# Kernel tuning notes

Measured on AMD Instinct MI355X. Metric: run time of the kernel, lower is better.

The kernel has to match this reference:

```python
import jax, jax.numpy as jnp
from jax import lax
import numpy as np

B, N, D = 2, 4096, 1024
D_INNER = 2 * D          # expand=2
D_STATE = 16
D_CONV = 4
DT_RANK = (D + 15) // 16 # ceil(d_model/16) = 64
EPS = 1e-6


def setup_inputs() -> dict:
    key = jax.random.key(0)
    ks = jax.random.split(key, 12)
    s = lambda k, shape, sc=0.02: jax.random.normal(k, shape, jnp.float32) * sc
    return {
        "x": jax.random.normal(ks[0], (B, N, D), jnp.float32),
        "c": jax.random.normal(ks[1], (B, D), jnp.float32),
        # LayerNorm(hidden_size, eps=1e-6)
        "ln_g": jnp.ones((D,), jnp.float32),
        "ln_b": jnp.zeros((D,), jnp.float32),
        # adaLN_modulation: SiLU -> Linear(D, 3D)
        "ada_w": s(ks[2], (3 * D, D)),
        "ada_b": jnp.zeros((3 * D,), jnp.float32),
        # Mamba params
        "in_w": s(ks[3], (2 * D_INNER, D)),                     # in_proj (no bias)
        "conv_w": s(ks[4], (D_INNER, 1, D_CONV), 0.1),          # depthwise causal conv
        "conv_b": jnp.zeros((D_INNER,), jnp.float32),
        "xproj_w": s(ks[5], (DT_RANK + 2 * D_STATE, D_INNER)),  # x_proj (no bias)
        "dt_w": s(ks[6], (D_INNER, DT_RANK), 0.1),              # dt_proj
        "dt_b": jnp.log(jnp.expm1(jnp.full((D_INNER,), 0.01, jnp.float32))),  # softplus^-1(0.01)
        "A_log": jnp.log(jnp.tile(jnp.arange(1, D_STATE + 1, dtype=jnp.float32), (D_INNER, 1))),
        "D_skip": jnp.ones((D_INNER,), jnp.float32),
        "out_w": s(ks[7], (D, D_INNER)),                        # out_proj (no bias)
    }


def _mamba(h, in_w, conv_w, conv_b, xproj_w, dt_w, dt_b, A_log, D_skip, out_w):
    Bsz = h.shape[0]
    xz = h @ in_w.T                                   # (B,N,2*Di)
    u, z = jnp.split(xz, 2, axis=-1)                  # (B,N,Di) each
    # causal depthwise conv over time
    u = u.transpose(0, 2, 1)                          # (B,Di,N)
    u = lax.conv_general_dilated(u, conv_w, (1,), [(D_CONV - 1, 0)],
                                 feature_group_count=D_INNER)
    u = jax.nn.silu(u + conv_b[None, :, None]).transpose(0, 2, 1)  # (B,N,Di)
    # input-dependent dt, B, C
    dbc = u @ xproj_w.T                               # (B,N,dt_rank+2S)
    dt = dbc[..., :DT_RANK]
    Bm = dbc[..., DT_RANK:DT_RANK + D_STATE]          # (B,N,S)
    Cm = dbc[..., DT_RANK + D_STATE:]                 # (B,N,S)
    dt = jax.nn.softplus(dt @ dt_w.T + dt_b)          # (B,N,Di)
    A = -jnp.exp(A_log)                               # (Di,S)

    def step(hst, inputs):
        dt_t, b_t, c_t, u_t = inputs                  # (B,Di),(B,S),(B,S),(B,Di)
        dA = jnp.exp(dt_t[..., None] * A)             # (B,Di,S)
        hst = dA * hst + (dt_t * u_t)[..., None] * b_t[:, None, :]
        y = jnp.einsum('bds,bs->bd', hst, c_t)
        return hst, y

    xs = (dt.transpose(1, 0, 2), Bm.transpose(1, 0, 2),
          Cm.transpose(1, 0, 2), u.transpose(1, 0, 2))
    h0 = jnp.zeros((Bsz, D_INNER, D_STATE), h.dtype)
    _, ys = lax.scan(step, h0, xs)                    # ys: (N,B,Di)
    y = ys.transpose(1, 0, 2) + u * D_skip            # D skip connection
    y = y * jax.nn.silu(z)                            # gate
    return y @ out_w.T                                # (B,N,D)


def reference(x, c, ln_g, ln_b, ada_w, ada_b, in_w, conv_w, conv_b,
              xproj_w, dt_w, dt_b, A_log, D_skip, out_w):
    # adaLN modulation
    mod = jax.nn.silu(c) @ ada_w.T + ada_b            # (B,3D)
    shift, scale, gate = jnp.split(mod, 3, axis=-1)
    # LayerNorm(eps=1e-6)
    mu = jnp.mean(x, axis=-1, keepdims=True)
    var = jnp.mean(jnp.square(x - mu), axis=-1, keepdims=True)
    h = (x - mu) * lax.rsqrt(var + EPS) * ln_g + ln_b
    # modulate
    h = h * (1.0 + scale[:, None, :]) + shift[:, None, :]
    # Mamba selective scan
    h = _mamba(h, in_w, conv_w, conv_b, xproj_w, dt_w, dt_b, A_log, D_skip, out_w)
    # gated residual
    return x + gate[:, None, :] * h
```

## Files before the change

### kernel.cpp

```cpp
#include <hip/hip_runtime.h>

typedef unsigned short u16;
typedef short s8v __attribute__((ext_vector_type(8)));
typedef short s4v __attribute__((ext_vector_type(4)));
typedef float f4v __attribute__((ext_vector_type(4)));

#define DEV __device__ __forceinline__

DEV float bf2f(u16 u) { union { unsigned i; float f; } x; x.i = ((unsigned)u) << 16; return x.f; }
DEV u16 f2bf(float f) {
  union { float f; unsigned i; } x; x.f = f;
  unsigned r = x.i + 0x7FFFu + ((x.i >> 16) & 1u);
  return (u16)(r >> 16);
}
DEV float sbf(short s) { return bf2f((u16)s); }
DEV float sigm(float v) { return 1.f / (1.f + __expf(-v)); }

DEV void gl_lds(const u16* g, u16* l) {
  __builtin_amdgcn_global_load_lds(
      (const __attribute__((address_space(1))) unsigned int*)g,
      (__attribute__((address_space(3))) unsigned int*)l, 16, 0, 0);
}

struct CvtArgs { const void* src[15]; u16* dst[15]; int n8[15]; };

__global__ __launch_bounds__(256)
void k_convert_all(CvtArgs a) {
  const int f32in = (((const unsigned*)a.src[2])[0] == 0x3F800000u);
#pragma unroll
  for (int s = 0; s < 15; ++s) {
    const int n8 = a.n8[s];
    const void* src = a.src[s];
    u16* dst = a.dst[s];
    for (int i = blockIdx.x * 256 + threadIdx.x; i < n8; i += gridDim.x * 256) {
      if (f32in) {
        const f4v* f = (const f4v*)src;
        f4v va = f[(size_t)i * 2], vb = f[(size_t)i * 2 + 1];
        s8v o;
#pragma unroll
        for (int e = 0; e < 4; ++e) { o[e] = (short)f2bf(va[e]); o[4 + e] = (short)f2bf(vb[e]); }
        *(s8v*)(dst + (size_t)i * 8) = o;
      } else {
        *(s8v*)(dst + (size_t)i * 8) = ((const s8v*)src)[i];
      }
    }
  }
}

__global__ __launch_bounds__(64)
void k_mod(const u16* __restrict__ c, const u16* __restrict__ ada_w,
           const u16* __restrict__ ada_b, float* __restrict__ mod) {
  int o = blockIdx.x;
  int b = o / 3072, col = o % 3072;
  int lane = threadIdx.x;
  float acc = 0.f;
  for (int k = lane; k < 1024; k += 64) {
    float cv = bf2f(c[b * 1024 + k]);
    acc += cv * sigm(cv) * bf2f(ada_w[(size_t)col * 1024 + k]);
  }
#pragma unroll
  for (int off = 1; off < 64; off <<= 1) acc += __shfl_xor(acc, off);
  if (lane == 0) mod[o] = acc + bf2f(ada_b[col]);
}

__global__ __launch_bounds__(256)
void k_ln(const u16* __restrict__ x, const u16* __restrict__ gw, const u16* __restrict__ bw,
          const float* __restrict__ mod, u16* __restrict__ h) {
  int m = blockIdx.x, tid = threadIdx.x;
  int b = m >> 12;
  s4v xv = *(const s4v*)(x + (size_t)m * 1024 + tid * 4);
  float v[4]; float sum = 0.f, sq = 0.f;
#pragma unroll
  for (int e = 0; e < 4; ++e) { v[e] = sbf(xv[e]); sum += v[e]; sq += v[e] * v[e]; }
#pragma unroll
  for (int off = 1; off < 64; off <<= 1) { sum += __shfl_xor(sum, off); sq += __shfl_xor(sq, off); }
  __shared__ float s1[4], s2[4];
  if ((tid & 63) == 0) { s1[tid >> 6] = sum; s2[tid >> 6] = sq; }
  __syncthreads();
  sum = s1[0] + s1[1] + s1[2] + s1[3];
  sq  = s2[0] + s2[1] + s2[2] + s2[3];
  float mu = sum * (1.f / 1024.f);
  float rs = rsqrtf(sq * (1.f / 1024.f) - mu * mu + 1e-6f);
  const float* mrow = mod + b * 3072;
  s4v o4;
#pragma unroll
  for (int e = 0; e < 4; ++e) {
    int col = tid * 4 + e;
    float hv = (v[e] - mu) * rs * sbf(gw[col]) + sbf(bw[col]);
    hv = hv * (1.f + mrow[1024 + col]) + mrow[col];
    o4[e] = (short)f2bf(hv);
  }
  *(s4v*)(h + (size_t)m * 1024 + tid * 4) = o4;
}

enum { EPI_SPLIT = 0, EPI_DT = 1, EPI_OUT = 2 };

template <int EPI>
__global__ __launch_bounds__(256)
void gemm_bt(const u16* __restrict__ A, const u16* __restrict__ W, int Kdim,
             u16* __restrict__ out0, u16* __restrict__ out1,
             const float* __restrict__ modp, const u16* __restrict__ xin,
             const u16* __restrict__ dtb, const unsigned* __restrict__ rawg) {
  __shared__ __align__(16) u16 As[128 * 32];
  __shared__ __align__(16) u16 Bs[128 * 32];
  const int tid = threadIdx.x;
  const int lane = tid & 63, wid = tid >> 6;
  const int tm = blockIdx.x * 128, tn = blockIdx.y * 128;
  const int wm = (wid >> 1) * 64, wn = (wid & 1) * 64;
  const int g = lane >> 4, r15 = lane & 15;
  const int r0 = tid >> 2, c0 = (tid & 3) << 3;
  int f32out = 0;
  if constexpr (EPI == EPI_OUT) f32out = (rawg[0] == 0x3F800000u);

  f4v zero = {0.f, 0.f, 0.f, 0.f};
  f4v acc[4][4];
#pragma unroll
  for (int i = 0; i < 4; ++i)
#pragma unroll
    for (int j = 0; j < 4; ++j) acc[i][j] = zero;

  for (int k0 = 0; k0 < Kdim; k0 += 32) {
    __syncthreads();
    gl_lds(A + (size_t)(tm + r0) * Kdim + k0 + c0, As + tid * 8);
    gl_lds(A + (size_t)(tm + r0 + 64) * Kdim + k0 + c0, As + 2048 + tid * 8);
    gl_lds(W + (size_t)(tn + r0) * Kdim + k0 + c0, Bs + tid * 8);
    gl_lds(W + (size_t)(tn + r0 + 64) * Kdim + k0 + c0, Bs + 2048 + tid * 8);
    __syncthreads();
    s8v af[4], bf[4];
#pragma unroll
    for (int f = 0; f < 4; ++f) {
      af[f] = *(const s8v*)(As + (wm + f * 16 + r15) * 32 + g * 8);
      bf[f] = *(const s8v*)(Bs + (wn + f * 16 + r15) * 32 + g * 8);
    }
#pragma unroll
    for (int i = 0; i < 4; ++i)
#pragma unroll
      for (int j = 0; j < 4; ++j)
        acc[i][j] = __builtin_amdgcn_mfma_f32_16x16x32_bf16(af[i], bf[j], acc[i][j], 0, 0, 0);
  }

#pragma unroll
  for (int i = 0; i < 4; ++i)
#pragma unroll
    for (int j = 0; j < 4; ++j)
#pragma unroll
      for (int r = 0; r < 4; ++r) {
        int m = tm + wm + i * 16 + g * 4 + r;
        int col = tn + wn + j * 16 + r15;
        float v = acc[i][j][r];
        if constexpr (EPI == EPI_SPLIT) {
          if (col < 2048) out0[(size_t)m * 2048 + col] = f2bf(v);
          else            out1[(size_t)m * 2048 + (col - 2048)] = f2bf(v);
        } else if constexpr (EPI == EPI_DT) {
          v += bf2f(dtb[col]);
          v = v > 20.f ? v : log1pf(__expf(v));
          out0[(size_t)m * 2048 + col] = f2bf(v);
        } else {
          int b = m >> 12;
          float gate = modp[b * 3072 + 2048 + col];
          float xv = bf2f(xin[(size_t)m * 1024 + col]);
          float res = xv + gate * v;
          if (f32out) ((float*)out0)[(size_t)m * 1024 + col] = res;
          else        out0[(size_t)m * 1024 + col] = f2bf(res);
        }
      }
}

__global__ __launch_bounds__(128)
void gemm_dbc(const u16* __restrict__ A, const u16* __restrict__ W,
              u16* __restrict__ dtin, float* __restrict__ bc) {
  __shared__ __align__(16) u16 As[32 * 32];
  __shared__ __align__(16) u16 Bs[96 * 32];
  const int tid = threadIdx.x;
  const int lane = tid & 63, wid = tid >> 6;
  const int tm = blockIdx.x * 32;
  const int g = lane >> 4, r15 = lane & 15;
  const int r0 = tid >> 2, c0 = (tid & 3) << 3;

  f4v zero = {0.f, 0.f, 0.f, 0.f};
  f4v acc[6];
#pragma unroll
  for (int j = 0; j < 6; ++j) acc[j] = zero;

  for (int k0 = 0; k0 < 2048; k0 += 32) {
    __syncthreads();
    gl_lds(A + (size_t)(tm + r0) * 2048 + k0 + c0, As + tid * 8);
    gl_lds(W + (size_t)r0 * 2048 + k0 + c0,        Bs + tid * 8);
    gl_lds(W + (size_t)(r0 + 32) * 2048 + k0 + c0, Bs + 1024 + tid * 8);
    gl_lds(W + (size_t)(r0 + 64) * 2048 + k0 + c0, Bs + 2048 + tid * 8);
    __syncthreads();
    s8v af = *(const s8v*)(As + (wid * 16 + r15) * 32 + g * 8);
    s8v bf[6];
#pragma unroll
    for (int f = 0; f < 6; ++f)
      bf[f] = *(const s8v*)(Bs + (f * 16 + r15) * 32 + g * 8);
#pragma unroll
    for (int j = 0; j < 6; ++j)
      acc[j] = __builtin_amdgcn_mfma_f32_16x16x32_bf16(af, bf[j], acc[j], 0, 0, 0);
  }

#pragma unroll
  for (int j = 0; j < 6; ++j)
#pragma unroll
    for (int r = 0; r < 4; ++r) {
      int m = tm + wid * 16 + g * 4 + r;
      int col = j * 16 + r15;
      float v = acc[j][r];
      if (col < 64) dtin[(size_t)m * 64 + col] = f2bf(v);
      else          bc[(size_t)m * 32 + (col - 64)] = v;
    }
}

#define TT 16
__global__ __launch_bounds__(256)
void k_conv(const u16* __restrict__ uraw, const u16* __restrict__ cw,
            const u16* __restrict__ cb, u16* __restrict__ uo) {
  const int b = blockIdx.y;
  const int t0 = blockIdx.x * TT;
  const int dbase = threadIdx.x * 8;
  const size_t rowbase = (size_t)b * 4096 + t0;

  s8v cwv[4];
#pragma unroll
  for (int q = 0; q < 4; ++q) cwv[q] = *(const s8v*)(cw + dbase * 4 + q * 8);
  float w[8][4];
#pragma unroll
  for (int e = 0; e < 8; ++e)
#pragma unroll
    for (int j = 0; j < 4; ++j) { int q = e * 4 + j; w[e][j] = sbf(cwv[q >> 3][q & 7]); }
  s8v cbv = *(const s8v*)(cb + dbase);
  float bias[8];
#pragma unroll
  for (int e = 0; e < 8; ++e) bias[e] = sbf(cbv[e]);

  s8v rows[TT + 3];
  const s8v zz = {0, 0, 0, 0, 0, 0, 0, 0};
#pragma unroll
  for (int r = 0; r < TT + 3; ++r) {
    int t = t0 - 3 + r;
    rows[r] = (t < 0) ? zz : *(const s8v*)(uraw + (rowbase - 3 + r) * 2048 + dbase);
  }

#pragma unroll
  for (int t = 0; t < TT; ++t) {
    float acc[8];
#pragma unroll
    for (int e = 0; e < 8; ++e) acc[e] = bias[e];
#pragma unroll
    for (int j = 0; j < 4; ++j) {
      s8v v = rows[t + j];
#pragma unroll
      for (int e = 0; e < 8; ++e) acc[e] = fmaf(sbf(v[e]), w[e][j], acc[e]);
    }
    s8v o;
#pragma unroll
    for (int e = 0; e < 8; ++e) { float s = acc[e]; o[e] = (short)f2bf(s * sigm(s)); }
    *(s8v*)(uo + (rowbase + t) * 2048 + dbase) = o;
  }
}

#define NC 32
#define CT 128

__global__ __launch_bounds__(256)
void scan_local(const u16* __restrict__ dt, const u16* __restrict__ u,
                const float* __restrict__ bc, const u16* __restrict__ A_log,
                float* __restrict__ P, float* __restrict__ F) {
  const int cch = blockIdx.x, b = blockIdx.z;
  const int tid = threadIdx.x;
  const int d = blockIdx.y * 256 + tid;
  __shared__ float lbc[CT * 32];
  const size_t mbase = (size_t)b * 4096 + (size_t)cch * CT;
  for (int i = tid; i < CT * 32; i += 256) lbc[i] = bc[mbase * 32 + i];
  float Ads[16];
#pragma unroll
  for (int s = 0; s < 16; ++s) Ads[s] = -__expf(bf2f(A_log[d * 16 + s]));
  float h[16];
#pragma unroll
  for (int s = 0; s < 16; ++s) h[s] = 0.f;
  float S = 0.f;
  __syncthreads();
  const u16* dtp = dt + mbase * 2048 + d;
  const u16* up  = u  + mbase * 2048 + d;
  for (int t = 0; t < CT; ++t) {
    float dtv = bf2f(dtp[(size_t)t * 2048]);
    float uv  = bf2f(up[(size_t)t * 2048]);
    float du = dtv * uv;
    S += dtv;
    float Bv[16];
    *(f4v*)&Bv[0]  = *(const f4v*)&lbc[t * 32 + 0];
    *(f4v*)&Bv[4]  = *(const f4v*)&lbc[t * 32 + 4];
    *(f4v*)&Bv[8]  = *(const f4v*)&lbc[t * 32 + 8];
    *(f4v*)&Bv[12] = *(const f4v*)&lbc[t * 32 + 12];
#pragma unroll
    for (int s = 0; s < 16; ++s) {
      float a = __expf(dtv * Ads[s]);
      h[s] = fmaf(a, h[s], du * Bv[s]);
    }
  }
  const size_t o = (((size_t)b * NC + cch) * 2048 + d) * 16;
#pragma unroll
  for (int q = 0; q < 4; ++q) {
    f4v fv, pv;
#pragma unroll
    for (int e = 0; e < 4; ++e) { fv[e] = h[q * 4 + e]; pv[e] = __expf(S * Ads[q * 4 + e]); }
    *(f4v*)&F[o + q * 4] = fv;
    *(f4v*)&P[o + q * 4] = pv;
  }
}

__global__ __launch_bounds__(256)
void scan_cross(float* __restrict__ P, float* __restrict__ F) {
  int tid = blockIdx.x * 256 + threadIdx.x;
  int b = tid >> 15, r = tid & 32767;
  float H = 0.f;
  for (int cc = 0; cc < NC; ++cc) {
    size_t o = (((size_t)b * NC + cc) << 15) + r;
    float Pv = P[o], Fv = F[o];
    F[o] = H;
    H = fmaf(Pv, H, Fv);
  }
}

__global__ __launch_bounds__(256)
void scan_final(const u16* __restrict__ dt, const u16* __restrict__ u,
                const float* __restrict__ bc, const u16* __restrict__ A_log,
                const float* __restrict__ Hin, const u16* __restrict__ z,
                const u16* __restrict__ Dskip, u16* __restrict__ Ain) {
  const int cch = blockIdx.x, b = blockIdx.z;
  const int tid = threadIdx.x;
  const int d = blockIdx.y * 256 + tid;
  __shared__ float lbc[CT * 32];
  const size_t mbase = (size_t)b * 4096 + (size_t)cch * CT;
  for (int i = tid; i < CT * 32; i += 256) lbc[i] = bc[mbase * 32 + i];
  float Ads[16];
#pragma unroll
  for (int s = 0; s < 16; ++s) Ads[s] = -__expf(bf2f(A_log[d * 16 + s]));
  float h[16];
  const size_t o = (((size_t)b * NC + cch) * 2048 + d) * 16;
#pragma unroll
  for (int q = 0; q < 4; ++q) {
    f4v hv = *(const f4v*)&Hin[o + q * 4];
#pragma unroll
    for (int e = 0; e < 4; ++e) h[q * 4 + e] = hv[e];
  }
  const float dsk = bf2f(Dskip[d]);
  __syncthreads();
  const u16* dtp = dt + mbase * 2048 + d;
  const u16* up  = u  + mbase * 2048 + d;
  const u16* zp  = z  + mbase * 2048 + d;
  u16* op = Ain + mbase * 2048 + d;
  for (int t = 0; t < CT; ++t) {
    float dtv = bf2f(dtp[(size_t)t * 2048]);
    float uv  = bf2f(up[(size_t)t * 2048]);
    float zv  = bf2f(zp[(size_t)t * 2048]);
    float du = dtv * uv;
    float Bv[16], Cv[16];
    *(f4v*)&Bv[0]  = *(const f4v*)&lbc[t * 32 + 0];
    *(f4v*)&Bv[4]  = *(const f4v*)&lbc[t * 32 + 4];
    *(f4v*)&Bv[8]  = *(const f4v*)&lbc[t * 32 + 8];
    *(f4v*)&Bv[12] = *(const f4v*)&lbc[t * 32 + 12];
    *(f4v*)&Cv[0]  = *(const f4v*)&lbc[t * 32 + 16];
    *(f4v*)&Cv[4]  = *(const f4v*)&lbc[t * 32 + 20];
    *(f4v*)&Cv[8]  = *(const f4v*)&lbc[t * 32 + 24];
    *(f4v*)&Cv[12] = *(const f4v*)&lbc[t * 32 + 28];
    float y = 0.f;
#pragma unroll
    for (int s = 0; s < 16; ++s) {
      float a = __expf(dtv * Ads[s]);
      h[s] = fmaf(a, h[s], du * Bv[s]);
      y = fmaf(h[s], Cv[s], y);
    }
    float zs = zv * sigm(zv);
    op[(size_t)t * 2048] = f2bf((y + uv * dsk) * zs);
  }
}

extern "C" void kernel_launch(void* const* d_in, const int* in_sizes, int n_in,
                              void* d_out, int out_size, void* d_ws, size_t ws_size,
                              hipStream_t stream) {
  u16* out = (u16*)d_out;

  char* ws = (char*)d_ws;
  size_t off = 0;
  auto alloc = [&](size_t bytes) { void* p = ws + off; off += (bytes + 255) & ~(size_t)255; return p; };
  u16* cv[15];
  for (int i = 0; i < 15; ++i) cv[i] = (u16*)alloc((size_t)in_sizes[i] * 2);
  float* mod   = (float*)alloc(2 * 3072 * 4);
  u16*   zbuf  = (u16*)  alloc((size_t)8192 * 2048 * 2);
  u16*   uraw  = (u16*)  alloc((size_t)8192 * 2048 * 2);
  u16*   uconv = (u16*)  alloc((size_t)8192 * 2048 * 2);
  u16*   dtin  = (u16*)  alloc((size_t)8192 * 64 * 2);
  float* bc    = (float*)alloc((size_t)8192 * 32 * 4);
  float* Pb    = (float*)alloc((size_t)2 * NC * 2048 * 16 * 4);
  float* Fb    = (float*)alloc((size_t)2 * NC * 2048 * 16 * 4);
  u16*   Ain   = (u16*)  alloc((size_t)8192 * 2048 * 2);
  u16*   hln   = Ain;
  u16*   dtbuf = uraw;

  CvtArgs ca;
  for (int i = 0; i < 15; ++i) { ca.src[i] = d_in[i]; ca.dst[i] = cv[i]; ca.n8[i] = in_sizes[i] / 8; }
  k_convert_all<<<2048, 256, 0, stream>>>(ca);

  const u16 *x = cv[0], *c = cv[1], *ada_w = cv[4],
            *ada_b = cv[5], *in_w = cv[6], *conv_w = cv[7], *conv_b = cv[8],
            *xproj = cv[9], *dt_w = cv[10], *dt_b = cv[11], *A_log = cv[12],
            *Dskip = cv[13], *out_w = cv[14];
  const u16 *ln_gb = cv[2], *ln_bb = cv[3];
  const unsigned* rawg = (const unsigned*)d_in[2];

  k_mod<<<6144, 64, 0, stream>>>(c, ada_w, ada_b, mod);
  k_ln<<<8192, 256, 0, stream>>>(x, ln_gb, ln_bb, mod, hln);
  gemm_bt<EPI_SPLIT><<<dim3(64, 32), 256, 0, stream>>>(hln, in_w, 1024, uraw, zbuf, nullptr, nullptr, nullptr, nullptr);
  k_conv<<<dim3(256, 2), 256, 0, stream>>>(uraw, conv_w, conv_b, uconv);
  gemm_dbc<<<256, 128, 0, stream>>>(uconv, xproj, dtin, bc);
  gemm_bt<EPI_DT><<<dim3(64, 16), 256, 0, stream>>>(dtin, dt_w, 64, dtbuf, nullptr, nullptr, nullptr, dt_b, nullptr);
  scan_local<<<dim3(NC, 8, 2), 256, 0, stream>>>(dtbuf, uconv, bc, A_log, Pb, Fb);
  scan_cross<<<256, 256, 0, stream>>>(Pb, Fb);
  scan_final<<<dim3(NC, 8, 2), 256, 0, stream>>>(dtbuf, uconv, bc, A_log, Fb, zbuf, Dskip, Ain);
  gemm_bt<EPI_OUT><<<dim3(64, 8), 256, 0, stream>>>(Ain, out_w, 2048, out, nullptr, mod, x, nullptr, rawg);
}
```

Baseline: 593.5 us.

## Double-buffer GEMM LDS tiles and read raw x directly instead of converting

Both MFMA GEMM kernels now use two LDS buffers, issuing the next K-tile's global-to-LDS loads before computing on the current tile, with one barrier per iteration instead of two. Separately, the conversion pass skips x, and the LayerNorm and output epilogue read the raw input (fp32 or bf16, detected from ln_g) directly. This removes an 8192x1024 conversion pass and overlaps load latency with MFMA work, at the cost of doubled LDS per block, which may reduce occupancy.

```diff
diff --git a/kernel.cpp b/kernel.cpp
--- a/kernel.cpp
+++ b/kernel.cpp
@@ -64,14 +64,25 @@
 }
 
 __global__ __launch_bounds__(256)
-void k_ln(const u16* __restrict__ x, const u16* __restrict__ gw, const u16* __restrict__ bw,
+void k_ln(const void* __restrict__ xraw, const unsigned* __restrict__ rawg,
+          const u16* __restrict__ gw, const u16* __restrict__ bw,
           const float* __restrict__ mod, u16* __restrict__ h) {
   int m = blockIdx.x, tid = threadIdx.x;
   int b = m >> 12;
-  s4v xv = *(const s4v*)(x + (size_t)m * 1024 + tid * 4);
-  float v[4]; float sum = 0.f, sq = 0.f;
-#pragma unroll
-  for (int e = 0; e < 4; ++e) { v[e] = sbf(xv[e]); sum += v[e]; sq += v[e] * v[e]; }
+  const int f32in = (rawg[0] == 0x3F800000u);
+  float v[4];
+  if (f32in) {
+    f4v xv = ((const f4v*)xraw)[(size_t)m * 256 + tid];
+#pragma unroll
+    for (int e = 0; e < 4; ++e) v[e] = xv[e];
+  } else {
+    s4v xv = ((const s4v*)xraw)[(size_t)m * 256 + tid];
+#pragma unroll
+    for (int e = 0; e < 4; ++e) v[e] = sbf(xv[e]);
+  }
+  float sum = 0.f, sq = 0.f;
+#pragma unroll
+  for (int e = 0; e < 4; ++e) { sum += v[e]; sq += v[e] * v[e]; }
 #pragma unroll
   for (int off = 1; off < 64; off <<= 1) { sum += __shfl_xor(sum, off); sq += __shfl_xor(sq, off); }
   __shared__ float s1[4], s2[4];
@@ -99,10 +110,10 @@
 __global__ __launch_bounds__(256)
 void gemm_bt(const u16* __restrict__ A, const u16* __restrict__ W, int Kdim,
              u16* __restrict__ out0, u16* __restrict__ out1,
-             const float* __restrict__ modp, const u16* __restrict__ xin,
+             const float* __restrict__ modp, const void* __restrict__ xin,
              const u16* __restrict__ dtb, const unsigned* __restrict__ rawg) {
-  __shared__ __align__(16) u16 As[128 * 32];
-  __shared__ __align__(16) u16 Bs[128 * 32];
+  __shared__ __align__(16) u16 As[2][128 * 32];
+  __shared__ __align__(16) u16 Bs[2][128 * 32];
   const int tid = threadIdx.x;
   const int lane = tid & 63, wid = tid >> 6;
   const int tm = blockIdx.x * 128, tn = blockIdx.y * 128;
@@ -112,6 +123,11 @@
   int f32out = 0;
   if constexpr (EPI == EPI_OUT) f32out = (rawg[0] == 0x3F800000u);
 
+  const u16* Ap  = A + (size_t)(tm + r0) * Kdim + c0;
+  const u16* Ap2 = A + (size_t)(tm + r0 + 64) * Kdim + c0;
+  const u16* Wp  = W + (size_t)(tn + r0) * Kdim + c0;
+  const u16* Wp2 = W + (size_t)(tn + r0 + 64) * Kdim + c0;
+
   f4v zero = {0.f, 0.f, 0.f, 0.f};
   f4v acc[4][4];
 #pragma unroll
@@ -119,24 +135,33 @@
 #pragma unroll
     for (int j = 0; j < 4; ++j) acc[i][j] = zero;
 
+  gl_lds(Ap, As[0] + tid * 8);
+  gl_lds(Ap2, As[0] + 2048 + tid * 8);
+  gl_lds(Wp, Bs[0] + tid * 8);
+  gl_lds(Wp2, Bs[0] + 2048 + tid * 8);
+  __syncthreads();
+
+  int cur = 0;
   for (int k0 = 0; k0 < Kdim; k0 += 32) {
-    __syncthreads();
-    gl_lds(A + (size_t)(tm + r0) * Kdim + k0 + c0, As + tid * 8);
-    gl_lds(A + (size_t)(tm + r0 + 64) * Kdim + k0 + c0, As + 2048 + tid * 8);
-    gl_lds(W + (size_t)(tn + r0) * Kdim + k0 + c0, Bs + tid * 8);
-    gl_lds(W + (size_t)(tn + r0 + 64) * Kdim + k0 + c0, Bs + 2048 + tid * 8);
-    __syncthreads();
+    if (k0 + 32 < Kdim) {
+      gl_lds(Ap + k0 + 32, As[cur ^ 1] + tid * 8);
+      gl_lds(Ap2 + k0 + 32, As[cur ^ 1] + 2048 + tid * 8);
+      gl_lds(Wp + k0 + 32, Bs[cur ^ 1] + tid * 8);
+      gl_lds(Wp2 + k0 + 32, Bs[cur ^ 1] + 2048 + tid * 8);
+    }
     s8v af[4], bf[4];
 #pragma unroll
     for (int f = 0; f < 4; ++f) {
-      af[f] = *(const s8v*)(As + (wm + f * 16 + r15) * 32 + g * 8);
-      bf[f] = *(const s8v*)(Bs + (wn + f * 16 + r15) * 32 + g * 8);
+      af[f] = *(const s8v*)(As[cur] + (wm + f * 16 + r15) * 32 + g * 8);
+      bf[f] = *(const s8v*)(Bs[cur] + (wn + f * 16 + r15) * 32 + g * 8);
     }
 #pragma unroll
     for (int i = 0; i < 4; ++i)
 #pragma unroll
       for (int j = 0; j < 4; ++j)
         acc[i][j] = __builtin_amdgcn_mfma_f32_16x16x32_bf16(af[i], bf[j], acc[i][j], 0, 0, 0);
+    __syncthreads();
+    cur ^= 1;
   }
 
 #pragma unroll
@@ -158,10 +183,11 @@
         } else {
           int b = m >> 12;
           float gate = modp[b * 3072 + 2048 + col];
-          float xv = bf2f(xin[(size_t)m * 1024 + col]);
+          size_t xi = (size_t)m * 1024 + col;
+          float xv = f32out ? ((const float*)xin)[xi] : bf2f(((const u16*)xin)[xi]);
           float res = xv + gate * v;
-          if (f32out) ((float*)out0)[(size_t)m * 1024 + col] = res;
-          else        out0[(size_t)m * 1024 + col] = f2bf(res);
+          if (f32out) ((float*)out0)[xi] = res;
+          else        out0[xi] = f2bf(res);
         }
       }
 }
@@ -169,34 +195,48 @@
 __global__ __launch_bounds__(128)
 void gemm_dbc(const u16* __restrict__ A, const u16* __restrict__ W,
               u16* __restrict__ dtin, float* __restrict__ bc) {
-  __shared__ __align__(16) u16 As[32 * 32];
-  __shared__ __align__(16) u16 Bs[96 * 32];
+  __shared__ __align__(16) u16 As[2][32 * 32];
+  __shared__ __align__(16) u16 Bs[2][96 * 32];
   const int tid = threadIdx.x;
   const int lane = tid & 63, wid = tid >> 6;
   const int tm = blockIdx.x * 32;
   const int g = lane >> 4, r15 = lane & 15;
   const int r0 = tid >> 2, c0 = (tid & 3) << 3;
 
+  const u16* Ap  = A + (size_t)(tm + r0) * 2048 + c0;
+  const u16* Wp  = W + (size_t)r0 * 2048 + c0;
+  const u16* Wp2 = W + (size_t)(r0 + 32) * 2048 + c0;
+  const u16* Wp3 = W + (size_t)(r0 + 64) * 2048 + c0;
+
   f4v zero = {0.f, 0.f, 0.f, 0.f};
   f4v acc[6];
 #pragma unroll
   for (int j = 0; j < 6; ++j) acc[j] = zero;
 
+  gl_lds(Ap, As[0] + tid * 8);
+  gl_lds(Wp, Bs[0] + tid * 8);
+  gl_lds(Wp2, Bs[0] + 1024 + tid * 8);
+  gl_lds(Wp3, Bs[0] + 2048 + tid * 8);
+  __syncthreads();
+
+  int cur = 0;
   for (int k0 = 0; k0 < 2048; k0 += 32) {
-    __syncthreads();
-    gl_lds(A + (size_t)(tm + r0) * 2048 + k0 + c0, As + tid * 8);
-    gl_lds(W + (size_t)r0 * 2048 + k0 + c0,        Bs + tid * 8);
-    gl_lds(W + (size_t)(r0 + 32) * 2048 + k0 + c0, Bs + 1024 + tid * 8);
-    gl_lds(W + (size_t)(r0 + 64) * 2048 + k0 + c0, Bs + 2048 + tid * 8);
-    __syncthreads();
-    s8v af = *(const s8v*)(As + (wid * 16 + r15) * 32 + g * 8);
+    if (k0 + 32 < 2048) {
+      gl_lds(Ap + k0 + 32, As[cur ^ 1] + tid * 8);
+      gl_lds(Wp + k0 + 32, Bs[cur ^ 1] + tid * 8);
+      gl_lds(Wp2 + k0 + 32, Bs[cur ^ 1] + 1024 + tid * 8);
+      gl_lds(Wp3 + k0 + 32, Bs[cur ^ 1] + 2048 + tid * 8);
+    }
+    s8v af = *(const s8v*)(As[cur] + (wid * 16 + r15) * 32 + g * 8);
     s8v bf[6];
 #pragma unroll
     for (int f = 0; f < 6; ++f)
-      bf[f] = *(const s8v*)(Bs + (f * 16 + r15) * 32 + g * 8);
+      bf[f] = *(const s8v*)(Bs[cur] + (f * 16 + r15) * 32 + g * 8);
 #pragma unroll
     for (int j = 0; j < 6; ++j)
       acc[j] = __builtin_amdgcn_mfma_f32_16x16x32_bf16(af, bf[j], acc[j], 0, 0, 0);
+    __syncthreads();
+    cur ^= 1;
   }
 
 #pragma unroll
@@ -400,17 +440,19 @@
 
   CvtArgs ca;
   for (int i = 0; i < 15; ++i) { ca.src[i] = d_in[i]; ca.dst[i] = cv[i]; ca.n8[i] = in_sizes[i] / 8; }
+  ca.n8[0] = 0;
   k_convert_all<<<2048, 256, 0, stream>>>(ca);
 
-  const u16 *x = cv[0], *c = cv[1], *ada_w = cv[4],
+  const u16 *c = cv[1], *ada_w = cv[4],
             *ada_b = cv[5], *in_w = cv[6], *conv_w = cv[7], *conv_b = cv[8],
             *xproj = cv[9], *dt_w = cv[10], *dt_b = cv[11], *A_log = cv[12],
             *Dskip = cv[13], *out_w = cv[14];
   const u16 *ln_gb = cv[2], *ln_bb = cv[3];
   const unsigned* rawg = (const unsigned*)d_in[2];
+  const void* xraw = d_in[0];
 
   k_mod<<<6144, 64, 0, stream>>>(c, ada_w, ada_b, mod);
-  k_ln<<<8192, 256, 0, stream>>>(x, ln_gb, ln_bb, mod, hln);
+  k_ln<<<8192, 256, 0, stream>>>(xraw, rawg, ln_gb, ln_bb, mod, hln);
   gemm_bt<EPI_SPLIT><<<dim3(64, 32), 256, 0, stream>>>(hln, in_w, 1024, uraw, zbuf, nullptr, nullptr, nullptr, nullptr);
   k_conv<<<dim3(256, 2), 256, 0, stream>>>(uraw, conv_w, conv_b, uconv);
   gemm_dbc<<<256, 128, 0, stream>>>(uconv, xproj, dtin, bc);
@@ -418,5 +460,5 @@
   scan_local<<<dim3(NC, 8, 2), 256, 0, stream>>>(dtbuf, uconv, bc, A_log, Pb, Fb);
   scan_cross<<<256, 256, 0, stream>>>(Pb, Fb);
   scan_final<<<dim3(NC, 8, 2), 256, 0, stream>>>(dtbuf, uconv, bc, A_log, Fb, zbuf, Dskip, Ain);
-  gemm_bt<EPI_OUT><<<dim3(64, 8), 256, 0, stream>>>(Ain, out_w, 2048, out, nullptr, mod, x, nullptr, rawg);
-}
+  gemm_bt<EPI_OUT><<<dim3(64, 8), 256, 0, stream>>>(Ain, out_w, 2048, out, nullptr, mod, xraw, nullptr, rawg);
+}
```

After: 586.3 us. No clear change (-1.2%).
